# Kernel tuning notes

Hardware: AMD Instinct MI355X
Metric: run time of the kernel (lower is better)

The kernel has to match this reference:

```python
import jax, jax.numpy as jnp
import numpy as np

B, N, D, D_OUT = 8, 2048, 256, 256
LN_EPS = 1e-5
LRELU_SLOPE = 0.01


def setup_inputs() -> dict:
    key = jax.random.key(0)
    ks = jax.random.split(key, 11)
    s_in = 1.0 / np.sqrt(D)
    s_out = 1.0 / np.sqrt(D)
    return {
        "x_local": jax.random.normal(ks[0], (B, N, D), dtype=jnp.float32),
        "Wq": jax.random.uniform(ks[1], (D, D), jnp.float32, -s_in, s_in),
        "bq": jax.random.uniform(ks[2], (D,), jnp.float32, -s_in, s_in),
        "Wk": jax.random.uniform(ks[3], (D, D), jnp.float32, -s_in, s_in),
        "bk": jax.random.uniform(ks[4], (D,), jnp.float32, -s_in, s_in),
        "Wv": jax.random.uniform(ks[5], (D, D), jnp.float32, -s_in, s_in),
        "bv": jax.random.uniform(ks[6], (D,), jnp.float32, -s_in, s_in),
        "Wo": jax.random.uniform(ks[7], (D_OUT, D), jnp.float32, -s_out, s_out),
        "bo": jax.random.uniform(ks[8], (D_OUT,), jnp.float32, -s_out, s_out),
        "ln_gamma": jnp.ones((D_OUT,), jnp.float32),
        "ln_beta": jnp.zeros((D_OUT,), jnp.float32),
    }


def reference(x_local, Wq, bq, Wk, bk, Wv, bv, Wo, bo, ln_gamma, ln_beta):
    # Linear layers (torch convention: y = x @ W.T + b)
    Q = jnp.einsum("bnd,ed->bne", x_local, Wq) + bq
    K = jnp.einsum("bnd,ed->bne", x_local, Wk) + bk
    V = jnp.einsum("bnd,ed->bne", x_local, Wv) + bv
    # Unscaled attention (source applies no 1/sqrt(d))
    scores = jnp.einsum("bnd,bmd->bnm", Q, K)          # [B, N, N]
    attn = jax.nn.softmax(scores, axis=-1)
    loc = jnp.einsum("bnm,bmd->bnd", attn, V)           # [B, N, D]
    # fc_out: Linear -> LayerNorm -> LeakyReLU
    h = jnp.einsum("bnd,ed->bne", loc, Wo) + bo          # [B, N, D_OUT]
    mu = jnp.mean(h, axis=-1, keepdims=True)
    var = jnp.mean(jnp.square(h - mu), axis=-1, keepdims=True)
    hn = (h - mu) / jnp.sqrt(var + LN_EPS) * ln_gamma + ln_beta
    return jnp.where(hn >= 0, hn, LRELU_SLOPE * hn)
```

## Files before the change

### kernel.cpp

```cpp
#include <hip/hip_runtime.h>

typedef unsigned short u16;
typedef __attribute__((ext_vector_type(8))) _Float16 f16x8;
typedef __attribute__((ext_vector_type(4))) float f32x4;

#define MFMA_F16 __builtin_amdgcn_mfma_f32_16x16x32_f16

static __device__ __forceinline__ u16 f2h(float f) {
    return __builtin_bit_cast(u16, (_Float16)f);
}
static __device__ __forceinline__ ushort4 f4_to_h4(const float4 v) {
    ushort4 r;
    r.x = f2h(v.x); r.y = f2h(v.y); r.z = f2h(v.z); r.w = f2h(v.w);
    return r;
}

__global__ __launch_bounds__(256) void prep_w(
    const float* __restrict__ wq, const float* __restrict__ wk,
    const float* __restrict__ wv, const float* __restrict__ wo,
    u16* __restrict__ w4)
{
    const int tid = blockIdx.x * 256 + threadIdx.x;
    for (int i = tid; i < 65536; i += 16384) {
        const float* src = (i < 16384) ? wq : (i < 32768) ? wk
                         : (i < 49152) ? wv : wo;
        ((ushort4*)w4)[i] = f4_to_h4(((const float4*)src)[i & 16383]);
    }
}

__global__ __launch_bounds__(256) void proj_qkv(
    const float* __restrict__ X, const u16* __restrict__ w4,
    const float* __restrict__ bq, const float* __restrict__ bk,
    const float* __restrict__ bv,
    u16* __restrict__ Qh, u16* __restrict__ Kh, u16* __restrict__ Vt)
{
    const int z = blockIdx.y;
    const u16* __restrict__ W     = w4 + z * 65536;
    const float* __restrict__ bias = (z == 0) ? bq : (z == 1) ? bk : bv;

    const int m0   = blockIdx.x * 64;
    const int t    = threadIdx.x;
    const int w    = t >> 6;
    const int lane = t & 63;
    const int quad = lane >> 4;
    const int l16  = lane & 15;

    __shared__ __align__(16) u16 smem[18432];
    u16* Xs = smem;
    u16* Ws = smem + 2560;

    f32x4 acc[16];
#pragma unroll
    for (int i = 0; i < 16; ++i) acc[i] = f32x4{0.f, 0.f, 0.f, 0.f};

    for (int kc = 0; kc < 8; ++kc) {
#pragma unroll
        for (int i = 0; i < 2; ++i) {
            const int ch = i * 256 + t;
            const int row = ch >> 3, cg = ch & 7;
            const float4 v = *(const float4*)&X[(size_t)(m0 + row) * 256 + kc * 32 + cg * 4];
            *(ushort4*)&Xs[row * 40 + cg * 4] = f4_to_h4(v);
        }
#pragma unroll
        for (int i = 0; i < 4; ++i) {
            const int ch = i * 256 + t;
            const int row = ch >> 2, cg = ch & 3;
            *(int4*)&Ws[row * 40 + cg * 8] =
                *(const int4*)&W[(size_t)row * 256 + kc * 32 + cg * 8];
        }
        __syncthreads();

        const f16x8 af = *(const f16x8*)&Xs[(w * 16 + l16) * 40 + quad * 8];
#pragma unroll
        for (int nt = 0; nt < 16; ++nt) {
            const f16x8 bf = *(const f16x8*)&Ws[(nt * 16 + l16) * 40 + quad * 8];
            acc[nt] = MFMA_F16(af, bf, acc[nt], 0, 0, 0);
        }
        __syncthreads();
    }

    if (z < 2) {
        u16* __restrict__ Y = (z == 0) ? Qh : Kh;
#pragma unroll
        for (int nt = 0; nt < 16; ++nt) {
            const int col = nt * 16 + l16;
            const float bb = bias[col];
#pragma unroll
            for (int r = 0; r < 4; ++r)
                smem[(w * 16 + quad * 4 + r) * 264 + col] = f2h(acc[nt][r] + bb);
        }
        __syncthreads();
#pragma unroll
        for (int i = 0; i < 8; ++i) {
            const int ch = i * 256 + t;
            const int row = ch >> 5, cg = ch & 31;
            *(int4*)&Y[(size_t)(m0 + row) * 256 + cg * 8] =
                *(const int4*)&smem[row * 264 + cg * 8];
        }
    } else {
        const int b  = m0 >> 11;
        const int n0 = m0 & 2047;
#pragma unroll
        for (int nt = 0; nt < 16; ++nt) {
            const int col = nt * 16 + l16;
            const float bb = bias[col];
            ushort4 h4;
            h4.x = f2h(acc[nt][0] + bb);
            h4.y = f2h(acc[nt][1] + bb);
            h4.z = f2h(acc[nt][2] + bb);
            h4.w = f2h(acc[nt][3] + bb);
            *(ushort4*)&smem[col * 72 + w * 16 + quad * 4] = h4;
        }
        __syncthreads();
#pragma unroll
        for (int i = 0; i < 8; ++i) {
            const int ch = i * 256 + t;
            const int row = ch >> 3, cg = ch & 7;
            *(int4*)&Vt[(size_t)b * 524288 + (size_t)row * 2048 + n0 + cg * 8] =
                *(const int4*)&smem[row * 72 + cg * 8];
        }
    }
}

__global__ __launch_bounds__(256) void attn(
    const u16* __restrict__ Qh, const u16* __restrict__ Kg,
    const u16* __restrict__ Vt, u16* __restrict__ Op, float* __restrict__ lmp)
{
    const int nz = gridDim.z;
    const int z  = blockIdx.z;
    const int tbase = 64 / nz, trem = 64 % nz;
    const int my_tiles = tbase + (z < trem ? 1 : 0);
    const int tile0    = tbase * z + (z < trem ? z : trem);

    const int b  = blockIdx.y;
    const int q0 = blockIdx.x * 64;
    const int t    = threadIdx.x;
    const int w    = t >> 6;
    const int lane = t & 63;
    const int quad = lane >> 4;
    const int l16  = lane & 15;

    __shared__ __align__(16) u16 smem[18688];
    u16* Ks = smem;
    u16* Vs = smem + 8448;
    u16* Os = smem;

    f16x8 qf[8];
    {
        const size_t qrow = (size_t)(b * 2048 + q0 + w * 16 + l16) * 256;
#pragma unroll
        for (int kc = 0; kc < 8; ++kc)
            qf[kc] = *(const f16x8*)&Qh[qrow + kc * 32 + quad * 8];
    }

    f32x4 O[16];
#pragma unroll
    for (int i = 0; i < 16; ++i) O[i] = f32x4{0.f, 0.f, 0.f, 0.f};
    float mrow = -1e30f, lrow = 0.f;

    for (int it = 0; it < my_tiles; ++it) {
        const int kt = (tile0 + it) * 32;
#pragma unroll
        for (int i = 0; i < 4; ++i) {
            const int ch = i * 256 + t;
            const int row = ch >> 5, cg = ch & 31;
            const int prow = ((row >> 2) & 3) * 8 + (row >> 4) * 4 + (row & 3);
            *(int4*)&Ks[row * 264 + cg * 8] =
                *(const int4*)&Kg[(size_t)(b * 2048 + kt + prow) * 256 + cg * 8];
        }
#pragma unroll
        for (int i = 0; i < 4; ++i) {
            const int ch = i * 256 + t;
            const int row = ch >> 2, cg = ch & 3;
            *(int4*)&Vs[row * 40 + cg * 8] =
                *(const int4*)&Vt[(size_t)b * 524288 + (size_t)row * 2048 + kt + cg * 8];
        }
        __syncthreads();

        f32x4 S[2];
        S[0] = f32x4{0.f, 0.f, 0.f, 0.f};
        S[1] = f32x4{0.f, 0.f, 0.f, 0.f};
#pragma unroll
        for (int kc = 0; kc < 8; ++kc) {
#pragma unroll
            for (int kn = 0; kn < 2; ++kn) {
                const f16x8 kf = *(const f16x8*)&Ks[(kn * 16 + l16) * 264 + kc * 32 + quad * 8];
                S[kn] = MFMA_F16(kf, qf[kc], S[kn], 0, 0, 0);
            }
        }

        float mt = fmaxf(fmaxf(fmaxf(S[0][0], S[0][1]), fmaxf(S[0][2], S[0][3])),
                         fmaxf(fmaxf(S[1][0], S[1][1]), fmaxf(S[1][2], S[1][3])));
        mt = fmaxf(mt, __shfl_xor(mt, 16));
        mt = fmaxf(mt, __shfl_xor(mt, 32));
        const float mnew = fmaxf(mrow, mt);
        const float a = __expf(mrow - mnew);
        float p[2][4];
        float s = 0.f;
#pragma unroll
        for (int kn = 0; kn < 2; ++kn)
#pragma unroll
            for (int r = 0; r < 4; ++r) {
                p[kn][r] = __expf(S[kn][r] - mnew);
                s += p[kn][r];
            }
        s += __shfl_xor(s, 16);
        s += __shfl_xor(s, 32);
        lrow = a * lrow + s;
        mrow = mnew;

        if (__any(a < 1.f)) {
#pragma unroll
            for (int dv = 0; dv < 16; ++dv)
#pragma unroll
                for (int r = 0; r < 4; ++r) O[dv][r] *= a;
        }

        f16x8 pf;
#pragma unroll
        for (int kn = 0; kn < 2; ++kn)
#pragma unroll
            for (int r = 0; r < 4; ++r)
                pf[kn * 4 + r] = (_Float16)p[kn][r];

#pragma unroll
        for (int dvt = 0; dvt < 16; ++dvt) {
            const f16x8 vf = *(const f16x8*)&Vs[(dvt * 16 + l16) * 40 + quad * 8];
            O[dvt] = MFMA_F16(vf, pf, O[dvt], 0, 0, 0);
        }
        __syncthreads();
    }

    {
        const float rl = 1.0f / lrow;
#pragma unroll
        for (int dvt = 0; dvt < 16; ++dvt) {
            ushort4 h4;
            h4.x = f2h(O[dvt][0] * rl);
            h4.y = f2h(O[dvt][1] * rl);
            h4.z = f2h(O[dvt][2] * rl);
            h4.w = f2h(O[dvt][3] * rl);
            *(ushort4*)&Os[(w * 16 + l16) * 264 + dvt * 16 + quad * 4] = h4;
        }
        if (quad == 0) {
            const int grow = b * 2048 + q0 + w * 16 + l16;
            lmp[z * 16384 + grow]        = lrow;
            lmp[(nz + z) * 16384 + grow] = mrow;
        }
    }
    __syncthreads();

    u16* __restrict__ Oz = Op + (size_t)z * 4194304;
    {
        const int row = t >> 2;
#pragma unroll
        for (int i = 0; i < 8; ++i) {
            const int chunk = (t & 3) * 8 + i;
            *(int4*)&Oz[(size_t)(b * 2048 + q0 + row) * 256 + chunk * 8] =
                *(const int4*)&Os[row * 264 + chunk * 8];
        }
    }
}

__global__ __launch_bounds__(256) void outproj_ln(
    const u16* __restrict__ Op, const float* __restrict__ lmp,
    const u16* __restrict__ Woh, const float* __restrict__ bo,
    const float* __restrict__ gamma, const float* __restrict__ beta,
    float* __restrict__ out)
{
    const int m0   = blockIdx.x * 64;
    const int t    = threadIdx.x;
    const int w    = t >> 6;
    const int lane = t & 63;
    const int quad = lane >> 4;
    const int l16  = lane & 15;

    __shared__ __align__(16) u16 Ls[64 * 40];
    __shared__ __align__(16) u16 Ws[256 * 40];
    __shared__ _Float16 w0s[64], w1s[64];

    if (t < 64) {
        const float l0 = lmp[m0 + t],          l1 = lmp[16384 + m0 + t];
        const float mm0 = lmp[32768 + m0 + t], mm1 = lmp[49152 + m0 + t];
        const float mm = fmaxf(mm0, mm1);
        const float u0 = l0 * __expf(mm0 - mm);
        const float u1 = l1 * __expf(mm1 - mm);
        const float inv = 1.0f / (u0 + u1);
        w0s[t] = (_Float16)(u0 * inv);
        w1s[t] = (_Float16)(u1 * inv);
    }
    __syncthreads();

    f32x4 acc[16];
#pragma unroll
    for (int i = 0; i < 16; ++i) acc[i] = f32x4{0.f, 0.f, 0.f, 0.f};

    for (int kc = 0; kc < 8; ++kc) {
        {
            const int row = t >> 2, cg = t & 3;
            const size_t off = (size_t)(m0 + row) * 256 + kc * 32 + cg * 8;
            const f16x8 o0 = __builtin_bit_cast(f16x8, *(const int4*)&Op[off]);
            const f16x8 o1 = __builtin_bit_cast(f16x8, *(const int4*)&Op[4194304 + off]);
            const _Float16 w0 = w0s[row], w1 = w1s[row];
            f16x8 lw;
#pragma unroll
            for (int j = 0; j < 8; ++j) lw[j] = o0[j] * w0 + o1[j] * w1;
            *(int4*)&Ls[row * 40 + cg * 8] = __builtin_bit_cast(int4, lw);
        }
#pragma unroll
        for (int i = 0; i < 4; ++i) {
            const int ch = i * 256 + t;
            const int row = ch >> 2, cg = ch & 3;
            *(int4*)&Ws[row * 40 + cg * 8] =
                *(const int4*)&Woh[(size_t)row * 256 + kc * 32 + cg * 8];
        }
        __syncthreads();

        const f16x8 af = *(const f16x8*)&Ls[(w * 16 + l16) * 40 + quad * 8];
#pragma unroll
        for (int nt = 0; nt < 16; ++nt) {
            const f16x8 bf = *(const f16x8*)&Ws[(nt * 16 + l16) * 40 + quad * 8];
            acc[nt] = MFMA_F16(af, bf, acc[nt], 0, 0, 0);
        }
        __syncthreads();
    }

    float g[16], bt[16], bb[16];
#pragma unroll
    for (int nt = 0; nt < 16; ++nt) {
        const int col = nt * 16 + l16;
        bb[nt] = bo[col]; g[nt] = gamma[col]; bt[nt] = beta[col];
    }

#pragma unroll
    for (int r = 0; r < 4; ++r) {
        float h[16];
        float sh = 0.f, sh2 = 0.f;
#pragma unroll
        for (int nt = 0; nt < 16; ++nt) {
            h[nt] = acc[nt][r] + bb[nt];
            sh  += h[nt];
            sh2 += h[nt] * h[nt];
        }
        sh  += __shfl_xor(sh, 1);  sh  += __shfl_xor(sh, 2);
        sh  += __shfl_xor(sh, 4);  sh  += __shfl_xor(sh, 8);
        sh2 += __shfl_xor(sh2, 1); sh2 += __shfl_xor(sh2, 2);
        sh2 += __shfl_xor(sh2, 4); sh2 += __shfl_xor(sh2, 8);
        const float mu  = sh * (1.f / 256.f);
        const float var = fmaxf(sh2 * (1.f / 256.f) - mu * mu, 0.f);
        const float rs  = rsqrtf(var + 1e-5f);
        const size_t row = (size_t)(m0 + w * 16 + quad * 4 + r) * 256;
#pragma unroll
        for (int nt = 0; nt < 16; ++nt) {
            const float hn = (h[nt] - mu) * rs * g[nt] + bt[nt];
            out[row + nt * 16 + l16] = (hn >= 0.f) ? hn : 0.01f * hn;
        }
    }
}

extern "C" void kernel_launch(void* const* d_in, const int* in_sizes, int n_in,
                              void* d_out, int out_size, void* d_ws, size_t ws_size,
                              hipStream_t stream)
{
    const float* x  = (const float*)d_in[0];
    const float* Wq = (const float*)d_in[1];
    const float* bq = (const float*)d_in[2];
    const float* Wk = (const float*)d_in[3];
    const float* bk = (const float*)d_in[4];
    const float* Wv = (const float*)d_in[5];
    const float* bv = (const float*)d_in[6];
    const float* Wo = (const float*)d_in[7];
    const float* bo = (const float*)d_in[8];
    const float* gm = (const float*)d_in[9];
    const float* bt = (const float*)d_in[10];
    float* out = (float*)d_out;

    u16* W4 = (u16*)d_ws;
    u16* Qh = W4 + 262144;
    u16* Kh = Qh + 4194304;
    u16* Vt = Kh + 4194304;
    u16* Op = Vt + 4194304;
    float* lmp = (float*)(Op + 2 * 4194304);
    u16* Woh = W4 + 196608;

    prep_w     <<<64,             256, 0, stream>>>(Wq, Wk, Wv, Wo, W4);
    proj_qkv   <<<dim3(256, 3),   256, 0, stream>>>(x, W4, bq, bk, bv, Qh, Kh, Vt);
    attn       <<<dim3(32, 8, 2), 256, 0, stream>>>(Qh, Kh, Vt, Op, lmp);
    outproj_ln <<<256,            256, 0, stream>>>(Op, lmp, Woh, bo, gm, bt, out);
}
```

Baseline: 199.3 us.

## Split attention KV range four ways with lazy rescaling and MFMA priority hints

Raises the attention split along the key dimension from two to four z-slices, doubling the number of attention blocks. The extra partial outputs are staged in the output buffer and the per-row l/m stats in the dead weight workspace, and outproj_ln merges four partials instead of two. Inside the loop, the online-softmax rescale now runs only when the running max grows by more than 8, and s_setprio is raised around the MFMA sections. The cost is more partial-output traffic in the merge step, plus reliance on buffer aliasing and on fp16 headroom for exponentials up to e^8.

```diff
diff --git a/kernel.cpp b/kernel.cpp
--- a/kernel.cpp
+++ b/kernel.cpp
@@ -124,7 +124,8 @@
 
 __global__ __launch_bounds__(256) void attn(
     const u16* __restrict__ Qh, const u16* __restrict__ Kg,
-    const u16* __restrict__ Vt, u16* __restrict__ Op, float* __restrict__ lmp)
+    const u16* __restrict__ Vt, u16* __restrict__ Op,
+    u16* __restrict__ OutS, float* __restrict__ lmpL, float* __restrict__ lmpM)
 {
     const int nz = gridDim.z;
     const int z  = blockIdx.z;
@@ -180,6 +181,7 @@
         f32x4 S[2];
         S[0] = f32x4{0.f, 0.f, 0.f, 0.f};
         S[1] = f32x4{0.f, 0.f, 0.f, 0.f};
+        __builtin_amdgcn_s_setprio(1);
 #pragma unroll
         for (int kc = 0; kc < 8; ++kc) {
 #pragma unroll
@@ -188,33 +190,34 @@
                 S[kn] = MFMA_F16(kf, qf[kc], S[kn], 0, 0, 0);
             }
         }
+        __builtin_amdgcn_s_setprio(0);
 
         float mt = fmaxf(fmaxf(fmaxf(S[0][0], S[0][1]), fmaxf(S[0][2], S[0][3])),
                          fmaxf(fmaxf(S[1][0], S[1][1]), fmaxf(S[1][2], S[1][3])));
         mt = fmaxf(mt, __shfl_xor(mt, 16));
         mt = fmaxf(mt, __shfl_xor(mt, 32));
-        const float mnew = fmaxf(mrow, mt);
-        const float a = __expf(mrow - mnew);
+        if (__any(mt - mrow > 8.f)) {
+            const float mnew = fmaxf(mrow, mt);
+            const float a = __expf(mrow - mnew);
+            lrow *= a;
+#pragma unroll
+            for (int dv = 0; dv < 16; ++dv)
+#pragma unroll
+                for (int r = 0; r < 4; ++r) O[dv][r] *= a;
+            mrow = mnew;
+        }
         float p[2][4];
         float s = 0.f;
 #pragma unroll
         for (int kn = 0; kn < 2; ++kn)
 #pragma unroll
             for (int r = 0; r < 4; ++r) {
-                p[kn][r] = __expf(S[kn][r] - mnew);
+                p[kn][r] = __expf(S[kn][r] - mrow);
                 s += p[kn][r];
             }
         s += __shfl_xor(s, 16);
         s += __shfl_xor(s, 32);
-        lrow = a * lrow + s;
-        mrow = mnew;
-
-        if (__any(a < 1.f)) {
-#pragma unroll
-            for (int dv = 0; dv < 16; ++dv)
-#pragma unroll
-                for (int r = 0; r < 4; ++r) O[dv][r] *= a;
-        }
+        lrow += s;
 
         f16x8 pf;
 #pragma unroll
@@ -223,11 +226,13 @@
             for (int r = 0; r < 4; ++r)
                 pf[kn * 4 + r] = (_Float16)p[kn][r];
 
+        __builtin_amdgcn_s_setprio(1);
 #pragma unroll
         for (int dvt = 0; dvt < 16; ++dvt) {
             const f16x8 vf = *(const f16x8*)&Vs[(dvt * 16 + l16) * 40 + quad * 8];
             O[dvt] = MFMA_F16(vf, pf, O[dvt], 0, 0, 0);
         }
+        __builtin_amdgcn_s_setprio(0);
         __syncthreads();
     }
 
@@ -244,26 +249,37 @@
         }
         if (quad == 0) {
             const int grow = b * 2048 + q0 + w * 16 + l16;
-            lmp[z * 16384 + grow]        = lrow;
-            lmp[(nz + z) * 16384 + grow] = mrow;
+            lmpL[z * 16384 + grow] = lrow;
+            lmpM[z * 16384 + grow] = mrow;
         }
     }
     __syncthreads();
 
-    u16* __restrict__ Oz = Op + (size_t)z * 4194304;
     {
         const int row = t >> 2;
-#pragma unroll
-        for (int i = 0; i < 8; ++i) {
-            const int chunk = (t & 3) * 8 + i;
-            *(int4*)&Oz[(size_t)(b * 2048 + q0 + row) * 256 + chunk * 8] =
-                *(const int4*)&Os[row * 264 + chunk * 8];
+        if (z < 2) {
+            u16* __restrict__ Oz = Op + (size_t)z * 4194304;
+#pragma unroll
+            for (int i = 0; i < 8; ++i) {
+                const int chunk = (t & 3) * 8 + i;
+                *(int4*)&Oz[(size_t)(b * 2048 + q0 + row) * 256 + chunk * 8] =
+                    *(const int4*)&Os[row * 264 + chunk * 8];
+            }
+        } else {
+            u16* __restrict__ Oz = OutS + (size_t)(z - 2) * 256;
+#pragma unroll
+            for (int i = 0; i < 8; ++i) {
+                const int chunk = (t & 3) * 8 + i;
+                *(int4*)&Oz[(size_t)(b * 2048 + q0 + row) * 512 + chunk * 8] =
+                    *(const int4*)&Os[row * 264 + chunk * 8];
+            }
         }
     }
 }
 
 __global__ __launch_bounds__(256) void outproj_ln(
-    const u16* __restrict__ Op, const float* __restrict__ lmp,
+    const u16* __restrict__ Op, const u16* __restrict__ OutS,
+    const float* __restrict__ lmpL, const float* __restrict__ lmpM,
     const u16* __restrict__ Woh, const float* __restrict__ bo,
     const float* __restrict__ gamma, const float* __restrict__ beta,
     float* __restrict__ out)
@@ -277,17 +293,23 @@
 
     __shared__ __align__(16) u16 Ls[64 * 40];
     __shared__ __align__(16) u16 Ws[256 * 40];
-    __shared__ _Float16 w0s[64], w1s[64];
+    __shared__ _Float16 wls[4][64];
 
     if (t < 64) {
-        const float l0 = lmp[m0 + t],          l1 = lmp[16384 + m0 + t];
-        const float mm0 = lmp[32768 + m0 + t], mm1 = lmp[49152 + m0 + t];
-        const float mm = fmaxf(mm0, mm1);
-        const float u0 = l0 * __expf(mm0 - mm);
-        const float u1 = l1 * __expf(mm1 - mm);
-        const float inv = 1.0f / (u0 + u1);
-        w0s[t] = (_Float16)(u0 * inv);
-        w1s[t] = (_Float16)(u1 * inv);
+        const float l0 = lmpL[m0 + t],         l1 = lmpL[16384 + m0 + t];
+        const float l2 = lmpL[32768 + m0 + t], l3 = lmpL[49152 + m0 + t];
+        const float m0v = lmpM[m0 + t],          m1v = lmpM[16384 + m0 + t];
+        const float m2v = lmpM[32768 + m0 + t],  m3v = lmpM[49152 + m0 + t];
+        const float mm = fmaxf(fmaxf(m0v, m1v), fmaxf(m2v, m3v));
+        const float u0 = l0 * __expf(m0v - mm);
+        const float u1 = l1 * __expf(m1v - mm);
+        const float u2 = l2 * __expf(m2v - mm);
+        const float u3 = l3 * __expf(m3v - mm);
+        const float inv = 1.0f / (u0 + u1 + u2 + u3);
+        wls[0][t] = (_Float16)(u0 * inv);
+        wls[1][t] = (_Float16)(u1 * inv);
+        wls[2][t] = (_Float16)(u2 * inv);
+        wls[3][t] = (_Float16)(u3 * inv);
     }
     __syncthreads();
 
@@ -298,13 +320,18 @@
     for (int kc = 0; kc < 8; ++kc) {
         {
             const int row = t >> 2, cg = t & 3;
-            const size_t off = (size_t)(m0 + row) * 256 + kc * 32 + cg * 8;
+            const size_t off  = (size_t)(m0 + row) * 256 + kc * 32 + cg * 8;
+            const size_t offS = (size_t)(m0 + row) * 512 + kc * 32 + cg * 8;
             const f16x8 o0 = __builtin_bit_cast(f16x8, *(const int4*)&Op[off]);
             const f16x8 o1 = __builtin_bit_cast(f16x8, *(const int4*)&Op[4194304 + off]);
-            const _Float16 w0 = w0s[row], w1 = w1s[row];
+            const f16x8 o2 = __builtin_bit_cast(f16x8, *(const int4*)&OutS[offS]);
+            const f16x8 o3 = __builtin_bit_cast(f16x8, *(const int4*)&OutS[offS + 256]);
+            const _Float16 w0 = wls[0][row], w1 = wls[1][row];
+            const _Float16 w2 = wls[2][row], w3 = wls[3][row];
             f16x8 lw;
 #pragma unroll
-            for (int j = 0; j < 8; ++j) lw[j] = o0[j] * w0 + o1[j] * w1;
+            for (int j = 0; j < 8; ++j)
+                lw[j] = o0[j] * w0 + o1[j] * w1 + o2[j] * w2 + o3[j] * w3;
             *(int4*)&Ls[row * 40 + cg * 8] = __builtin_bit_cast(int4, lw);
         }
 #pragma unroll
@@ -380,11 +407,13 @@
     u16* Kh = Qh + 4194304;
     u16* Vt = Kh + 4194304;
     u16* Op = Vt + 4194304;
-    float* lmp = (float*)(Op + 2 * 4194304);
+    float* lmpM = (float*)(Op + 2 * 4194304);
+    float* lmpL = (float*)W4;
     u16* Woh = W4 + 196608;
+    u16* OutS = (u16*)d_out;
 
     prep_w     <<<64,             256, 0, stream>>>(Wq, Wk, Wv, Wo, W4);
     proj_qkv   <<<dim3(256, 3),   256, 0, stream>>>(x, W4, bq, bk, bv, Qh, Kh, Vt);
-    attn       <<<dim3(32, 8, 2), 256, 0, stream>>>(Qh, Kh, Vt, Op, lmp);
-    outproj_ln <<<256,            256, 0, stream>>>(Op, lmp, Woh, bo, gm, bt, out);
-}
+    attn       <<<dim3(32, 8, 4), 256, 0, stream>>>(Qh, Kh, Vt, Op, OutS, lmpL, lmpM);
+    outproj_ln <<<256,            256, 0, stream>>>(Op, OutS, lmpL, lmpM, Woh, bo, gm, bt, out);
+}
```

New measurement: 194.2 us. 1.03x faster.

## Use 64-key tiles in attention with lazy rescale and MFMA priority hints

Applied to the files above, without the earlier changes.

Doubles the key/value tile per iteration from 32 to 64, halving the loop trip count and barrier count per block, and widens shared memory to hold the larger K and V tiles. Adds a lazy online-softmax rescale that only updates the running max and rescales O when the new max exceeds the old by more than 8. Wraps the MFMA sections in s_setprio raises. The larger shared footprint may reduce occupancy, and the split now assumes nz divides 32 evenly, dropping the remainder handling.

```diff
diff --git a/kernel.cpp b/kernel.cpp
--- a/kernel.cpp
+++ b/kernel.cpp
@@ -128,9 +128,8 @@
 {
     const int nz = gridDim.z;
     const int z  = blockIdx.z;
-    const int tbase = 64 / nz, trem = 64 % nz;
-    const int my_tiles = tbase + (z < trem ? 1 : 0);
-    const int tile0    = tbase * z + (z < trem ? z : trem);
+    const int ntiles = 32 / nz;
+    const int tile0  = ntiles * z;
 
     const int b  = blockIdx.y;
     const int q0 = blockIdx.x * 64;
@@ -140,9 +139,9 @@
     const int quad = lane >> 4;
     const int l16  = lane & 15;
 
-    __shared__ __align__(16) u16 smem[18688];
+    __shared__ __align__(16) u16 smem[35328];
     u16* Ks = smem;
-    u16* Vs = smem + 8448;
+    u16* Vs = smem + 16896;
     u16* Os = smem;
 
     f16x8 qf[8];
@@ -158,76 +157,87 @@
     for (int i = 0; i < 16; ++i) O[i] = f32x4{0.f, 0.f, 0.f, 0.f};
     float mrow = -1e30f, lrow = 0.f;
 
-    for (int it = 0; it < my_tiles; ++it) {
-        const int kt = (tile0 + it) * 32;
-#pragma unroll
-        for (int i = 0; i < 4; ++i) {
+    for (int it = 0; it < ntiles; ++it) {
+        const int kt = (tile0 + it) * 64;
+#pragma unroll
+        for (int i = 0; i < 8; ++i) {
             const int ch = i * 256 + t;
             const int row = ch >> 5, cg = ch & 31;
-            const int prow = ((row >> 2) & 3) * 8 + (row >> 4) * 4 + (row & 3);
+            const int prow = ((row >> 2) & 3) * 8 + ((row >> 4) & 1) * 4
+                           + (row & 3) + (row & 32);
             *(int4*)&Ks[row * 264 + cg * 8] =
                 *(const int4*)&Kg[(size_t)(b * 2048 + kt + prow) * 256 + cg * 8];
         }
 #pragma unroll
-        for (int i = 0; i < 4; ++i) {
-            const int ch = i * 256 + t;
-            const int row = ch >> 2, cg = ch & 3;
-            *(int4*)&Vs[row * 40 + cg * 8] =
+        for (int i = 0; i < 8; ++i) {
+            const int ch = i * 256 + t;
+            const int row = ch >> 3, cg = ch & 7;
+            *(int4*)&Vs[row * 72 + cg * 8] =
                 *(const int4*)&Vt[(size_t)b * 524288 + (size_t)row * 2048 + kt + cg * 8];
         }
         __syncthreads();
 
-        f32x4 S[2];
-        S[0] = f32x4{0.f, 0.f, 0.f, 0.f};
-        S[1] = f32x4{0.f, 0.f, 0.f, 0.f};
+        f32x4 S[4];
+#pragma unroll
+        for (int kn = 0; kn < 4; ++kn) S[kn] = f32x4{0.f, 0.f, 0.f, 0.f};
+        __builtin_amdgcn_s_setprio(1);
 #pragma unroll
         for (int kc = 0; kc < 8; ++kc) {
 #pragma unroll
-            for (int kn = 0; kn < 2; ++kn) {
+            for (int kn = 0; kn < 4; ++kn) {
                 const f16x8 kf = *(const f16x8*)&Ks[(kn * 16 + l16) * 264 + kc * 32 + quad * 8];
                 S[kn] = MFMA_F16(kf, qf[kc], S[kn], 0, 0, 0);
             }
         }
-
-        float mt = fmaxf(fmaxf(fmaxf(S[0][0], S[0][1]), fmaxf(S[0][2], S[0][3])),
-                         fmaxf(fmaxf(S[1][0], S[1][1]), fmaxf(S[1][2], S[1][3])));
+        __builtin_amdgcn_s_setprio(0);
+
+        float mt = -1e30f;
+#pragma unroll
+        for (int kn = 0; kn < 4; ++kn)
+            mt = fmaxf(mt, fmaxf(fmaxf(S[kn][0], S[kn][1]), fmaxf(S[kn][2], S[kn][3])));
         mt = fmaxf(mt, __shfl_xor(mt, 16));
         mt = fmaxf(mt, __shfl_xor(mt, 32));
-        const float mnew = fmaxf(mrow, mt);
-        const float a = __expf(mrow - mnew);
-        float p[2][4];
+        if (__any(mt - mrow > 8.f)) {
+            const float mnew = fmaxf(mrow, mt);
+            const float a = __expf(mrow - mnew);
+            lrow *= a;
+#pragma unroll
+            for (int dv = 0; dv < 16; ++dv)
+#pragma unroll
+                for (int r = 0; r < 4; ++r) O[dv][r] *= a;
+            mrow = mnew;
+        }
+        float p[4][4];
         float s = 0.f;
 #pragma unroll
-        for (int kn = 0; kn < 2; ++kn)
+        for (int kn = 0; kn < 4; ++kn)
 #pragma unroll
             for (int r = 0; r < 4; ++r) {
-                p[kn][r] = __expf(S[kn][r] - mnew);
+                p[kn][r] = __expf(S[kn][r] - mrow);
                 s += p[kn][r];
             }
         s += __shfl_xor(s, 16);
         s += __shfl_xor(s, 32);
-        lrow = a * lrow + s;
-        mrow = mnew;
-
-        if (__any(a < 1.f)) {
-#pragma unroll
-            for (int dv = 0; dv < 16; ++dv)
-#pragma unroll
-                for (int r = 0; r < 4; ++r) O[dv][r] *= a;
-        }
-
-        f16x8 pf;
+        lrow += s;
+
+        f16x8 pf0, pf1;
 #pragma unroll
         for (int kn = 0; kn < 2; ++kn)
 #pragma unroll
-            for (int r = 0; r < 4; ++r)
-                pf[kn * 4 + r] = (_Float16)p[kn][r];
-
+            for (int r = 0; r < 4; ++r) {
+                pf0[kn * 4 + r] = (_Float16)p[kn][r];
+                pf1[kn * 4 + r] = (_Float16)p[kn + 2][r];
+            }
+
+        __builtin_amdgcn_s_setprio(1);
 #pragma unroll
         for (int dvt = 0; dvt < 16; ++dvt) {
-            const f16x8 vf = *(const f16x8*)&Vs[(dvt * 16 + l16) * 40 + quad * 8];
-            O[dvt] = MFMA_F16(vf, pf, O[dvt], 0, 0, 0);
-        }
+            const f16x8 vf0 = *(const f16x8*)&Vs[(dvt * 16 + l16) * 72 + quad * 8];
+            O[dvt] = MFMA_F16(vf0, pf0, O[dvt], 0, 0, 0);
+            const f16x8 vf1 = *(const f16x8*)&Vs[(dvt * 16 + l16) * 72 + 32 + quad * 8];
+            O[dvt] = MFMA_F16(vf1, pf1, O[dvt], 0, 0, 0);
+        }
+        __builtin_amdgcn_s_setprio(0);
         __syncthreads();
     }
 
```

Measured after the change: 214.7 us. 7.7% more time.
